# Performance work log

Measured on AMD Instinct MI355X. Metric: run time of the kernel, lower is better.

Reference implementation:

```python
import jax, jax.numpy as jnp
import numpy as np

B, S, H, M = 8, 128, 768, 128
EPS = 1e-12


def setup_inputs() -> dict:
    key = jax.random.key(0)
    ks = jax.random.split(key, 8)
    seq_hiddens = jax.random.normal(ks[0], (B, S, H), dtype=jnp.float32)
    gamma = jnp.ones((H,), jnp.float32)
    beta = jnp.zeros((H,), jnp.float32)
    # conditional LN dense weights (torch Linear weight: (out, in)); small init so math stays stable
    w_beta = jax.random.normal(ks[1], (H, H), dtype=jnp.float32) * 0.02
    w_gamma = jax.random.normal(ks[2], (H, H), dtype=jnp.float32) * 0.02
    w_ent = jax.random.normal(ks[3], (H, M), dtype=jnp.float32) * 0.02
    w_head = jax.random.normal(ks[4], (H, M), dtype=jnp.float32) * 0.02
    w_tail = jax.random.normal(ks[5], (H, M), dtype=jnp.float32) * 0.02
    b_ent = jnp.zeros((M,), jnp.float32)
    b_head = jnp.zeros((M,), jnp.float32)
    b_tail = jnp.zeros((M,), jnp.float32)
    return dict(seq_hiddens=seq_hiddens, gamma=gamma, beta=beta, w_beta=w_beta,
                w_gamma=w_gamma, w_ent=w_ent, b_ent=b_ent, w_head=w_head,
                b_head=b_head, w_tail=w_tail, b_tail=b_tail)


def _handshake_cln(seq, gamma, beta, w_beta, w_gamma):
    # Triangular pair expansion in the same row-major order as the torch loop:
    # for ind in range(S): pairs (ind, ind), (ind, ind+1), ..., (ind, S-1)
    s = seq.shape[1]
    ii, jj = jnp.triu_indices(s)                 # (P,) each, P = S(S+1)/2
    x = seq[:, jj, :]                            # visible hiddens   (B, P, H)
    cond = seq[:, ii, :]                         # repeated hiddens  (B, P, H)
    beta_c = jnp.einsum('bph,oh->bpo', cond, w_beta) + beta      # (B, P, H)
    gamma_c = jnp.einsum('bph,oh->bpo', cond, w_gamma) + gamma   # (B, P, H)
    mean = jnp.mean(x, axis=-1, keepdims=True)
    out = x - mean
    var = jnp.mean(out * out, axis=-1, keepdims=True)
    std = (var + EPS) ** 2                       # NOTE: faithful to source (no sqrt)
    return out / std * gamma_c + beta_c


def reference(seq_hiddens, gamma, beta, w_beta, w_gamma, w_ent, b_ent,
              w_head, b_head, w_tail, b_tail):
    shaking = _handshake_cln(seq_hiddens, gamma, beta, w_beta, w_gamma)  # (B, P, H)
    ent = jnp.tanh(shaking @ w_ent + b_ent)      # (B, P, M)
    head = jnp.tanh(shaking @ w_head + b_head)
    tail = jnp.tanh(shaking @ w_tail + b_tail)
    return jnp.stack([ent, head, tail], axis=0)  # (3, B, P, M)
```

## Files before the change

### kernel.cpp

```cpp
#include <hip/hip_runtime.h>
#include <hip/hip_bf16.h>
#include <hip/hip_fp16.h>
#include <math.h>

#define B_   8
#define S_   128
#define H_   768
#define M_   128
#define P_   8256
#define BP_  66048
#define EPSF 1e-12f

typedef unsigned short u16;
typedef unsigned int   u32;
typedef _Float16 h16;
typedef _Float16 ffrag __attribute__((ext_vector_type(8)));
typedef float    f32x4 __attribute__((ext_vector_type(4)));

__device__ __forceinline__ u32 fuse2(u32 x, u32 g, u32 b) {
    __half2 r = __hfma2(__builtin_bit_cast(__half2, x),
                        __builtin_bit_cast(__half2, g),
                        __builtin_bit_cast(__half2, b));
    return __builtin_bit_cast(u32, r);
}
__device__ __forceinline__ float fast_tanh(float v) {
    float t = __expf(v + v);
    float r = __builtin_amdgcn_rcpf(t + 1.0f);
    return fmaf(-2.0f, r, 1.0f);
}
__device__ __forceinline__ void gl_lds16(const h16* g, h16* l) {
    __builtin_amdgcn_global_load_lds(
        (const __attribute__((address_space(1))) u32*)g,
        (__attribute__((address_space(3))) u32*)l, 16, 0, 0);
}

__global__ void k_prep(const float* __restrict__ seq,
                       const float* __restrict__ wg, const float* __restrict__ wb,
                       const float* __restrict__ we, const float* __restrict__ wh,
                       const float* __restrict__ wt,
                       const float* __restrict__ be, const float* __restrict__ bh,
                       const float* __restrict__ bt,
                       h16* __restrict__ wgb, h16* __restrict__ wbb,
                       h16* __restrict__ wct, float* __restrict__ biasc,
                       h16* __restrict__ xn, h16* __restrict__ condb)
{
    __shared__ float red[4];
    const int bx = blockIdx.x;
    const int t = threadIdx.x;

    if (bx < 5763) {
        int idx = bx * 256 + t;
        if (idx < 589824) {
            wgb[idx] = (h16)wg[idx];
        } else if (idx < 1179648) {
            int i = idx - 589824;
            wbb[i] = (h16)wb[i];
        } else if (idx < 1474560) {
            int i = idx - 1179648;
            int n = i / 768, h = i - n * 768;
            const float* w = (n < 128) ? we : (n < 256 ? wh : wt);
            wct[i] = (h16)w[h * 128 + (n & 127)];
        } else if (idx < 1474944) {
            int n = idx - 1474560;
            biasc[n] = (n < 128) ? be[n] : (n < 256 ? bh[n - 128] : bt[n - 256]);
        }
        return;
    }
    const int row = bx - 5763;
    const int lane = t & 63, wid = t >> 6;
    const float* x = seq + (size_t)row * H_;
    float x0 = x[t], x1 = x[t + 256], x2 = x[t + 512];

    float s = x0 + x1 + x2;
    for (int o = 32; o; o >>= 1) s += __shfl_xor(s, o);
    if (lane == 0) red[wid] = s;
    __syncthreads();
    float mean = (red[0] + red[1] + red[2] + red[3]) * (1.0f / 768.0f);

    float c0 = x0 - mean, c1 = x1 - mean, c2 = x2 - mean;
    float ss = c0 * c0 + c1 * c1 + c2 * c2;
    for (int o = 32; o; o >>= 1) ss += __shfl_xor(ss, o);
    __syncthreads();
    if (lane == 0) red[wid] = ss;
    __syncthreads();
    float var = (red[0] + red[1] + red[2] + red[3]) * (1.0f / 768.0f);
    float sd = var + EPSF;
    float scale = 1.0f / (sd * sd);

    h16* xr = xn + (size_t)row * H_;
    h16* cr = condb + (size_t)row * H_;
    xr[t] = (h16)(c0 * scale); xr[t + 256] = (h16)(c1 * scale); xr[t + 512] = (h16)(c2 * scale);
    cr[t] = (h16)x0;           cr[t + 256] = (h16)x1;           cr[t + 512] = (h16)x2;
}

__global__ __launch_bounds__(256) void k_cond_gemm(
    const h16* __restrict__ Ab, const h16* __restrict__ Wg, const h16* __restrict__ Wb,
    const float* __restrict__ gamma, const float* __restrict__ beta,
    h16* __restrict__ Gc, h16* __restrict__ Bc)
{
    __shared__ h16 Ash[64 * 72];
    __shared__ h16 Bsh[64 * 72];
    const int t = threadIdx.x;
    const int row0 = blockIdx.x * 64;
    const int by = blockIdx.y;
    const bool isg = (by < 12);
    const int nc0 = (isg ? by : by - 12) * 64;
    const h16* wsrc = isg ? Wg : Wb;

    const int r = t >> 2, q = t & 3;
    const h16* ap = Ab + (size_t)(row0 + r) * H_ + q * 16;
    const h16* wp = wsrc + (size_t)(nc0 + r) * H_ + q * 16;
    h16* asto = &Ash[r * 72 + q * 16];
    h16* bsto = &Bsh[r * 72 + q * 16];

    const int lane = t & 63, wid = t >> 6;
    const int wm0 = (wid >> 1) * 32, wn0 = (wid & 1) * 32;
    const int l15 = lane & 15, quad = lane >> 4, q8 = quad * 8;

    f32x4 acc[2][2] = {};
    for (int kt = 0; kt < 12; ++kt) {
        const int k0 = kt * 64;
        uint4 a0 = *(const uint4*)(ap + k0); uint4 a1 = *(const uint4*)(ap + k0 + 8);
        uint4 w0 = *(const uint4*)(wp + k0); uint4 w1 = *(const uint4*)(wp + k0 + 8);
        *(uint4*)asto = a0; *(uint4*)(asto + 8) = a1;
        *(uint4*)bsto = w0; *(uint4*)(bsto + 8) = w1;
        __syncthreads();
#pragma unroll
        for (int ks = 0; ks < 64; ks += 32) {
            ffrag af[2], bf[2];
#pragma unroll
            for (int mi = 0; mi < 2; ++mi)
                af[mi] = *reinterpret_cast<const ffrag*>(&Ash[(wm0 + mi * 16 + l15) * 72 + ks + q8]);
#pragma unroll
            for (int ni = 0; ni < 2; ++ni)
                bf[ni] = *reinterpret_cast<const ffrag*>(&Bsh[(wn0 + ni * 16 + l15) * 72 + ks + q8]);
#pragma unroll
            for (int mi = 0; mi < 2; ++mi)
#pragma unroll
                for (int ni = 0; ni < 2; ++ni)
                    acc[mi][ni] = __builtin_amdgcn_mfma_f32_16x16x32_f16(af[mi], bf[ni], acc[mi][ni], 0, 0, 0);
        }
        __syncthreads();
    }

    const float* bias = isg ? gamma : beta;
    h16* outp = isg ? Gc : Bc;
#pragma unroll
    for (int mi = 0; mi < 2; ++mi)
#pragma unroll
        for (int ni = 0; ni < 2; ++ni) {
            int c = wn0 + ni * 16 + l15;
            float bv = bias[nc0 + c];
#pragma unroll
            for (int reg = 0; reg < 4; ++reg) {
                int rg = wm0 + mi * 16 + quad * 4 + reg;
                outp[(size_t)(row0 + rg) * H_ + nc0 + c] = (h16)(acc[mi][ni][reg] + bv);
            }
        }
}

__global__ __launch_bounds__(256, 2) void k_pair_gemm(
    const h16* __restrict__ Xn, const h16* __restrict__ Gcb, const h16* __restrict__ Bcb,
    const h16* __restrict__ WcT, const float* __restrict__ biasc,
    float* __restrict__ out)
{
    __shared__ h16 Ash[2][4 * 128 * 8];
    __shared__ h16 Bsh[2][4 * 192 * 8];
    __shared__ int offx[128];
    __shared__ int offc[128];

    const int t = threadIdx.x;
    const int row0 = blockIdx.x * 128;
    const int nb = blockIdx.y;

    if (t < 128) {
        int gp = row0 + t;
        int b = gp / P_;
        int p = gp - b * P_;
        int i = (int)((257.0f - sqrtf(66049.0f - 8.0f * (float)p)) * 0.5f);
        if (i < 0) i = 0; if (i > 127) i = 127;
        while (i > 0 && (i * (257 - i)) / 2 > p) --i;
        while (((i + 1) * (256 - i)) / 2 <= p) ++i;
        int j = i + (p - (i * (257 - i)) / 2);
        offx[t] = b * 128 + j;
        offc[t] = b * 128 + i;
    }
    __syncthreads();

    const int r = t >> 1, half = t & 1;
    const h16* xp  = Xn  + (size_t)offx[r] * H_ + half * 16;
    const h16* gp_ = Gcb + (size_t)offc[r] * H_ + half * 16;
    const h16* bp_ = Bcb + (size_t)offc[r] * H_ + half * 16;
    const int aw0 = ((2 * half) * 128 + r) * 8;
    const int aw1 = ((2 * half + 1) * 128 + r) * 8;

    const h16* wbase = WcT + (size_t)nb * 192 * H_;
    const int wud = t & ~63;
    const h16* dsrc[3];
#pragma unroll
    for (int c = 0; c < 3; ++c) {
        int L = c * 256 + t;
        int ch = L / 192, n = L - ch * 192;
        dsrc[c] = wbase + (size_t)n * H_ + ch * 8;
    }

    const int lane = t & 63, wid = t >> 6;
    const int wm0 = (wid >> 1) * 64, wn0 = (wid & 1) * 96;
    const int l15 = lane & 15, quad = lane >> 4;

#pragma unroll
    for (int c = 0; c < 3; ++c)
        gl_lds16(dsrc[c], &Bsh[0][(c * 256 + wud) * 8]);
    {
        uint4 xa = *(const uint4*)xp;   uint4 xb = *(const uint4*)(xp + 8);
        uint4 ga = *(const uint4*)gp_;  uint4 gb = *(const uint4*)(gp_ + 8);
        uint4 ba = *(const uint4*)bp_;  uint4 bb = *(const uint4*)(bp_ + 8);
        uint4 f0, f1;
        f0.x = fuse2(xa.x, ga.x, ba.x); f0.y = fuse2(xa.y, ga.y, ba.y);
        f0.z = fuse2(xa.z, ga.z, ba.z); f0.w = fuse2(xa.w, ga.w, ba.w);
        f1.x = fuse2(xb.x, gb.x, bb.x); f1.y = fuse2(xb.y, gb.y, bb.y);
        f1.z = fuse2(xb.z, gb.z, bb.z); f1.w = fuse2(xb.w, gb.w, bb.w);
        *(uint4*)&Ash[0][aw0] = f0; *(uint4*)&Ash[0][aw1] = f1;
    }
    __syncthreads();

    f32x4 acc[4][6] = {};
#pragma unroll 2
    for (int kt = 0; kt < 24; ++kt) {
        const int buf = kt & 1, nbf = buf ^ 1;
        uint4 xa, xb, ga, gb, ba, bb;
        if (kt < 23) {
            const int k0 = (kt + 1) * 32;
#pragma unroll
            for (int c = 0; c < 3; ++c)
                gl_lds16(dsrc[c] + k0, &Bsh[nbf][(c * 256 + wud) * 8]);
            xa = *(const uint4*)(xp + k0);  xb = *(const uint4*)(xp + k0 + 8);
            ga = *(const uint4*)(gp_ + k0); gb = *(const uint4*)(gp_ + k0 + 8);
            ba = *(const uint4*)(bp_ + k0); bb = *(const uint4*)(bp_ + k0 + 8);
        }

        ffrag af[4], bf[6];
#pragma unroll
        for (int mi = 0; mi < 4; ++mi)
            af[mi] = *reinterpret_cast<const ffrag*>(&Ash[buf][(quad * 128 + wm0 + mi * 16 + l15) * 8]);
#pragma unroll
        for (int ni = 0; ni < 6; ++ni)
            bf[ni] = *reinterpret_cast<const ffrag*>(&Bsh[buf][(quad * 192 + wn0 + ni * 16 + l15) * 8]);
#pragma unroll
        for (int mi = 0; mi < 4; ++mi)
#pragma unroll
            for (int ni = 0; ni < 6; ++ni)
                acc[mi][ni] = __builtin_amdgcn_mfma_f32_16x16x32_f16(af[mi], bf[ni], acc[mi][ni], 0, 0, 0);

        if (kt < 23) {
            uint4 f0, f1;
            f0.x = fuse2(xa.x, ga.x, ba.x); f0.y = fuse2(xa.y, ga.y, ba.y);
            f0.z = fuse2(xa.z, ga.z, ba.z); f0.w = fuse2(xa.w, ga.w, ba.w);
            f1.x = fuse2(xb.x, gb.x, bb.x); f1.y = fuse2(xb.y, gb.y, bb.y);
            f1.z = fuse2(xb.z, gb.z, bb.z); f1.w = fuse2(xb.w, gb.w, bb.w);
            *(uint4*)&Ash[nbf][aw0] = f0; *(uint4*)&Ash[nbf][aw1] = f1;
        }
        __syncthreads();
    }

#pragma unroll
    for (int mi = 0; mi < 4; ++mi)
#pragma unroll
        for (int ni = 0; ni < 6; ++ni) {
            int cg = nb * 192 + wn0 + ni * 16 + l15;
            int head = cg >> 7, m = cg & 127;
            float bv = biasc[cg];
#pragma unroll
            for (int reg = 0; reg < 4; ++reg) {
                int rg = wm0 + mi * 16 + quad * 4 + reg;
                out[((size_t)head * BP_ + row0 + rg) * M_ + m] = fast_tanh(acc[mi][ni][reg] + bv);
            }
        }
}

extern "C" void kernel_launch(void* const* d_in, const int* in_sizes, int n_in,
                              void* d_out, int out_size, void* d_ws, size_t ws_size,
                              hipStream_t stream)
{
    const float* seq     = (const float*)d_in[0];
    const float* gamma   = (const float*)d_in[1];
    const float* beta    = (const float*)d_in[2];
    const float* w_beta  = (const float*)d_in[3];
    const float* w_gamma = (const float*)d_in[4];
    const float* w_ent   = (const float*)d_in[5];
    const float* b_ent   = (const float*)d_in[6];
    const float* w_head  = (const float*)d_in[7];
    const float* b_head  = (const float*)d_in[8];
    const float* w_tail  = (const float*)d_in[9];
    const float* b_tail  = (const float*)d_in[10];
    float* out = (float*)d_out;

    char* ws = (char*)d_ws;
    h16* xn    = (h16*)ws; ws += (size_t)1024 * 768 * 2;
    h16* condb = (h16*)ws; ws += (size_t)1024 * 768 * 2;
    h16* wgb   = (h16*)ws; ws += (size_t)768 * 768 * 2;
    h16* wbb   = (h16*)ws; ws += (size_t)768 * 768 * 2;
    h16* wct   = (h16*)ws; ws += (size_t)384 * 768 * 2;
    h16* gc    = (h16*)ws; ws += (size_t)1024 * 768 * 2;
    h16* bc    = (h16*)ws; ws += (size_t)1024 * 768 * 2;
    float* biasc = (float*)ws; ws += 384 * 4;

    hipLaunchKernelGGL(k_prep, dim3(5763 + 1024), dim3(256), 0, stream,
                       seq, w_gamma, w_beta, w_ent, w_head, w_tail,
                       b_ent, b_head, b_tail, wgb, wbb, wct, biasc, xn, condb);
    hipLaunchKernelGGL(k_cond_gemm, dim3(16, 24), dim3(256), 0, stream,
                       condb, wgb, wbb, gamma, beta, gc, bc);
    hipLaunchKernelGGL(k_pair_gemm, dim3(516, 2), dim3(256), 0, stream,
                       xn, gc, bc, wct, biasc, out);
}
```

Baseline: 234.5 us.

## Halve pair-GEMM row tile to 64 and transpose head weights via LDS

The pair GEMM now uses 64-row tiles, with each of the four waves covering 48 output columns. The grid doubles and launch bounds rise to allow three blocks per CU, which should improve occupancy and load balance across the 256 CUs. In the prep kernel, the strided gather transpose of the head weights is replaced by a 64x64 LDS-tiled transpose so that global reads and writes are coalesced. The cost is less reuse of each B tile and more redundant loads of the weight tiles.

```diff
diff --git a/kernel.cpp b/kernel.cpp
--- a/kernel.cpp
+++ b/kernel.cpp
@@ -34,6 +34,9 @@
         (__attribute__((address_space(3))) u32*)l, 16, 0, 0);
 }
 
+#define CONVN 4610
+#define WCT0  4610
+#define NORM0 4682
 __global__ void k_prep(const float* __restrict__ seq,
                        const float* __restrict__ wg, const float* __restrict__ wb,
                        const float* __restrict__ we, const float* __restrict__ wh,
@@ -45,28 +48,46 @@
                        h16* __restrict__ xn, h16* __restrict__ condb)
 {
     __shared__ float red[4];
+    __shared__ float tile[64][65];
     const int bx = blockIdx.x;
     const int t = threadIdx.x;
 
-    if (bx < 5763) {
+    if (bx < CONVN) {
         int idx = bx * 256 + t;
         if (idx < 589824) {
             wgb[idx] = (h16)wg[idx];
         } else if (idx < 1179648) {
             int i = idx - 589824;
             wbb[i] = (h16)wb[i];
-        } else if (idx < 1474560) {
-            int i = idx - 1179648;
-            int n = i / 768, h = i - n * 768;
-            const float* w = (n < 128) ? we : (n < 256 ? wh : wt);
-            wct[i] = (h16)w[h * 128 + (n & 127)];
-        } else if (idx < 1474944) {
-            int n = idx - 1474560;
+        } else if (idx < 1180032) {
+            int n = idx - 1179648;
             biasc[n] = (n < 128) ? be[n] : (n < 256 ? bh[n - 128] : bt[n - 256]);
         }
         return;
     }
-    const int row = bx - 5763;
+    if (bx < NORM0) {
+        int b = bx - WCT0;
+        int x = b / 24, rem = b - x * 24;
+        int mt = rem / 12, ht = rem - mt * 12;
+        int m0 = mt * 64, h0 = ht * 64;
+        const float* w = (x == 0) ? we : (x == 1 ? wh : wt);
+        int mm = t & 63, hh4 = t >> 6;
+#pragma unroll
+        for (int r2 = 0; r2 < 16; ++r2) {
+            int hh = hh4 + r2 * 4;
+            tile[hh][mm] = w[(size_t)(h0 + hh) * 128 + m0 + mm];
+        }
+        __syncthreads();
+        int hh2 = t & 63, nn4 = t >> 6;
+#pragma unroll
+        for (int r2 = 0; r2 < 16; ++r2) {
+            int nn = nn4 + r2 * 4;
+            int n = x * 128 + m0 + nn;
+            wct[(size_t)n * H_ + h0 + hh2] = (h16)tile[hh2][nn];
+        }
+        return;
+    }
+    const int row = bx - NORM0;
     const int lane = t & 63, wid = t >> 6;
     const float* x = seq + (size_t)row * H_;
     float x0 = x[t], x1 = x[t + 256], x2 = x[t + 512];
@@ -159,21 +180,21 @@
         }
 }
 
-__global__ __launch_bounds__(256, 2) void k_pair_gemm(
+__global__ __launch_bounds__(256, 3) void k_pair_gemm(
     const h16* __restrict__ Xn, const h16* __restrict__ Gcb, const h16* __restrict__ Bcb,
     const h16* __restrict__ WcT, const float* __restrict__ biasc,
     float* __restrict__ out)
 {
-    __shared__ h16 Ash[2][4 * 128 * 8];
+    __shared__ h16 Ash[2][4 * 64 * 8];
     __shared__ h16 Bsh[2][4 * 192 * 8];
-    __shared__ int offx[128];
-    __shared__ int offc[128];
+    __shared__ int offx[64];
+    __shared__ int offc[64];
 
     const int t = threadIdx.x;
-    const int row0 = blockIdx.x * 128;
+    const int row0 = blockIdx.x * 64;
     const int nb = blockIdx.y;
 
-    if (t < 128) {
+    if (t < 64) {
         int gp = row0 + t;
         int b = gp / P_;
         int p = gp - b * P_;
@@ -187,12 +208,11 @@
     }
     __syncthreads();
 
-    const int r = t >> 1, half = t & 1;
-    const h16* xp  = Xn  + (size_t)offx[r] * H_ + half * 16;
-    const h16* gp_ = Gcb + (size_t)offc[r] * H_ + half * 16;
-    const h16* bp_ = Bcb + (size_t)offc[r] * H_ + half * 16;
-    const int aw0 = ((2 * half) * 128 + r) * 8;
-    const int aw1 = ((2 * half + 1) * 128 + r) * 8;
+    const int r = t >> 2, c4 = t & 3;
+    const h16* xp  = Xn  + (size_t)offx[r] * H_ + c4 * 8;
+    const h16* gp_ = Gcb + (size_t)offc[r] * H_ + c4 * 8;
+    const h16* bp_ = Bcb + (size_t)offc[r] * H_ + c4 * 8;
+    const int aw = (c4 * 64 + r) * 8;
 
     const h16* wbase = WcT + (size_t)nb * 192 * H_;
     const int wud = t & ~63;
@@ -205,60 +225,56 @@
     }
 
     const int lane = t & 63, wid = t >> 6;
-    const int wm0 = (wid >> 1) * 64, wn0 = (wid & 1) * 96;
+    const int wn0 = wid * 48;
     const int l15 = lane & 15, quad = lane >> 4;
 
 #pragma unroll
     for (int c = 0; c < 3; ++c)
         gl_lds16(dsrc[c], &Bsh[0][(c * 256 + wud) * 8]);
     {
-        uint4 xa = *(const uint4*)xp;   uint4 xb = *(const uint4*)(xp + 8);
-        uint4 ga = *(const uint4*)gp_;  uint4 gb = *(const uint4*)(gp_ + 8);
-        uint4 ba = *(const uint4*)bp_;  uint4 bb = *(const uint4*)(bp_ + 8);
-        uint4 f0, f1;
-        f0.x = fuse2(xa.x, ga.x, ba.x); f0.y = fuse2(xa.y, ga.y, ba.y);
-        f0.z = fuse2(xa.z, ga.z, ba.z); f0.w = fuse2(xa.w, ga.w, ba.w);
-        f1.x = fuse2(xb.x, gb.x, bb.x); f1.y = fuse2(xb.y, gb.y, bb.y);
-        f1.z = fuse2(xb.z, gb.z, bb.z); f1.w = fuse2(xb.w, gb.w, bb.w);
-        *(uint4*)&Ash[0][aw0] = f0; *(uint4*)&Ash[0][aw1] = f1;
-    }
-    __syncthreads();
-
-    f32x4 acc[4][6] = {};
+        uint4 xa = *(const uint4*)xp;
+        uint4 ga = *(const uint4*)gp_;
+        uint4 ba = *(const uint4*)bp_;
+        uint4 f;
+        f.x = fuse2(xa.x, ga.x, ba.x); f.y = fuse2(xa.y, ga.y, ba.y);
+        f.z = fuse2(xa.z, ga.z, ba.z); f.w = fuse2(xa.w, ga.w, ba.w);
+        *(uint4*)&Ash[0][aw] = f;
+    }
+    __syncthreads();
+
+    f32x4 acc[4][3] = {};
 #pragma unroll 2
     for (int kt = 0; kt < 24; ++kt) {
         const int buf = kt & 1, nbf = buf ^ 1;
-        uint4 xa, xb, ga, gb, ba, bb;
+        uint4 xa, ga, ba;
         if (kt < 23) {
             const int k0 = (kt + 1) * 32;
 #pragma unroll
             for (int c = 0; c < 3; ++c)
                 gl_lds16(dsrc[c] + k0, &Bsh[nbf][(c * 256 + wud) * 8]);
-            xa = *(const uint4*)(xp + k0);  xb = *(const uint4*)(xp + k0 + 8);
-            ga = *(const uint4*)(gp_ + k0); gb = *(const uint4*)(gp_ + k0 + 8);
-            ba = *(const uint4*)(bp_ + k0); bb = *(const uint4*)(bp_ + k0 + 8);
-        }
-
-        ffrag af[4], bf[6];
+            xa = *(const uint4*)(xp + k0);
+            ga = *(const uint4*)(gp_ + k0);
+            ba = *(const uint4*)(bp_ + k0);
+        }
+
+        ffrag af[4], bf[3];
 #pragma unroll
         for (int mi = 0; mi < 4; ++mi)
-            af[mi] = *reinterpret_cast<const ffrag*>(&Ash[buf][(quad * 128 + wm0 + mi * 16 + l15) * 8]);
-#pragma unroll
-        for (int ni = 0; ni < 6; ++ni)
+            af[mi] = *reinterpret_cast<const ffrag*>(&Ash[buf][(quad * 64 + mi * 16 + l15) * 8]);
+#pragma unroll
+        for (int ni = 0; ni < 3; ++ni)
             bf[ni] = *reinterpret_cast<const ffrag*>(&Bsh[buf][(quad * 192 + wn0 + ni * 16 + l15) * 8]);
 #pragma unroll
         for (int mi = 0; mi < 4; ++mi)
 #pragma unroll
-            for (int ni = 0; ni < 6; ++ni)
+            for (int ni = 0; ni < 3; ++ni)
                 acc[mi][ni] = __builtin_amdgcn_mfma_f32_16x16x32_f16(af[mi], bf[ni], acc[mi][ni], 0, 0, 0);
 
         if (kt < 23) {
-            uint4 f0, f1;
-            f0.x = fuse2(xa.x, ga.x, ba.x); f0.y = fuse2(xa.y, ga.y, ba.y);
-            f0.z = fuse2(xa.z, ga.z, ba.z); f0.w = fuse2(xa.w, ga.w, ba.w);
-            f1.x = fuse2(xb.x, gb.x, bb.x); f1.y = fuse2(xb.y, gb.y, bb.y);
-            f1.z = fuse2(xb.z, gb.z, bb.z); f1.w = fuse2(xb.w, gb.w, bb.w);
-            *(uint4*)&Ash[nbf][aw0] = f0; *(uint4*)&Ash[nbf][aw1] = f1;
+            uint4 f;
+            f.x = fuse2(xa.x, ga.x, ba.x); f.y = fuse2(xa.y, ga.y, ba.y);
+            f.z = fuse2(xa.z, ga.z, ba.z); f.w = fuse2(xa.w, ga.w, ba.w);
+            *(uint4*)&Ash[nbf][aw] = f;
         }
         __syncthreads();
     }
@@ -266,13 +282,13 @@
 #pragma unroll
     for (int mi = 0; mi < 4; ++mi)
 #pragma unroll
-        for (int ni = 0; ni < 6; ++ni) {
+        for (int ni = 0; ni < 3; ++ni) {
             int cg = nb * 192 + wn0 + ni * 16 + l15;
             int head = cg >> 7, m = cg & 127;
             float bv = biasc[cg];
 #pragma unroll
             for (int reg = 0; reg < 4; ++reg) {
-                int rg = wm0 + mi * 16 + quad * 4 + reg;
+                int rg = mi * 16 + quad * 4 + reg;
                 out[((size_t)head * BP_ + row0 + rg) * M_ + m] = fast_tanh(acc[mi][ni][reg] + bv);
             }
         }
@@ -305,11 +321,11 @@
     h16* bc    = (h16*)ws; ws += (size_t)1024 * 768 * 2;
     float* biasc = (float*)ws; ws += 384 * 4;
 
-    hipLaunchKernelGGL(k_prep, dim3(5763 + 1024), dim3(256), 0, stream,
+    hipLaunchKernelGGL(k_prep, dim3(NORM0 + 1024), dim3(256), 0, stream,
                        seq, w_gamma, w_beta, w_ent, w_head, w_tail,
                        b_ent, b_head, b_tail, wgb, wbb, wct, biasc, xn, condb);
     hipLaunchKernelGGL(k_cond_gemm, dim3(16, 24), dim3(256), 0, stream,
                        condb, wgb, wbb, gamma, beta, gc, bc);
-    hipLaunchKernelGGL(k_pair_gemm, dim3(516, 2), dim3(256), 0, stream,
+    hipLaunchKernelGGL(k_pair_gemm, dim3(1032, 2), dim3(256), 0, stream,
                        xn, gc, bc, wct, biasc, out);
 }
```

Result: slower. 250.3 us (+6.7%).

## Pre-pack output weights into tile order and shrink pair-GEMM row tile

Applied to the files above, without the earlier changes.

The head weights are now pre-packed in the prep kernel into a tile-contiguous layout, so each k-step's weight tile is one contiguous 24KB chunk loaded straight to LDS. The pair GEMM switches from 128x192 tiles with K-step 32 to 64x192 tiles with K-step 64, doubling the grid to 1032x2 blocks and halving the k-loop trips. The aim is more blocks for occupancy and load balance on the GPU, plus fewer barriers and simpler weight addressing. The cost is that each weight tile is reused by fewer rows, so weight traffic per output row roughly doubles.

```diff
diff --git a/kernel.cpp b/kernel.cpp
--- a/kernel.cpp
+++ b/kernel.cpp
@@ -34,6 +34,7 @@
         (__attribute__((address_space(3))) u32*)l, 16, 0, 0);
 }
 
+#define NORM0 5763
 __global__ void k_prep(const float* __restrict__ seq,
                        const float* __restrict__ wg, const float* __restrict__ wb,
                        const float* __restrict__ we, const float* __restrict__ wh,
@@ -41,14 +42,14 @@
                        const float* __restrict__ be, const float* __restrict__ bh,
                        const float* __restrict__ bt,
                        h16* __restrict__ wgb, h16* __restrict__ wbb,
-                       h16* __restrict__ wct, float* __restrict__ biasc,
+                       h16* __restrict__ wpk, float* __restrict__ biasc,
                        h16* __restrict__ xn, h16* __restrict__ condb)
 {
     __shared__ float red[4];
     const int bx = blockIdx.x;
     const int t = threadIdx.x;
 
-    if (bx < 5763) {
+    if (bx < NORM0) {
         int idx = bx * 256 + t;
         if (idx < 589824) {
             wgb[idx] = (h16)wg[idx];
@@ -57,16 +58,26 @@
             wbb[i] = (h16)wb[i];
         } else if (idx < 1474560) {
             int i = idx - 1179648;
-            int n = i / 768, h = i - n * 768;
-            const float* w = (n < 128) ? we : (n < 256 ? wh : wt);
-            wct[i] = (h16)w[h * 128 + (n & 127)];
+            int e  = i & 7;
+            int u  = i >> 3;
+            int n  = u % 192;
+            int v  = u / 192;
+            int ch = v & 7;
+            int w2 = v >> 3;
+            int kt = w2 % 12;
+            int nb = w2 / 12;
+            int h  = kt * 64 + ch * 8 + e;
+            int ng = nb * 192 + n;
+            int head = ng >> 7, m = ng & 127;
+            const float* src = (head == 0) ? we : (head == 1 ? wh : wt);
+            wpk[i] = (h16)src[h * 128 + m];
         } else if (idx < 1474944) {
             int n = idx - 1474560;
             biasc[n] = (n < 128) ? be[n] : (n < 256 ? bh[n - 128] : bt[n - 256]);
         }
         return;
     }
-    const int row = bx - 5763;
+    const int row = bx - NORM0;
     const int lane = t & 63, wid = t >> 6;
     const float* x = seq + (size_t)row * H_;
     float x0 = x[t], x1 = x[t + 256], x2 = x[t + 512];
@@ -161,19 +172,19 @@
 
 __global__ __launch_bounds__(256, 2) void k_pair_gemm(
     const h16* __restrict__ Xn, const h16* __restrict__ Gcb, const h16* __restrict__ Bcb,
-    const h16* __restrict__ WcT, const float* __restrict__ biasc,
+    const h16* __restrict__ Wpk, const float* __restrict__ biasc,
     float* __restrict__ out)
 {
-    __shared__ h16 Ash[2][4 * 128 * 8];
-    __shared__ h16 Bsh[2][4 * 192 * 8];
-    __shared__ int offx[128];
-    __shared__ int offc[128];
+    __shared__ h16 Ash[2][8 * 64 * 8];
+    __shared__ h16 Bsh[2][8 * 192 * 8];
+    __shared__ int offx[64];
+    __shared__ int offc[64];
 
     const int t = threadIdx.x;
-    const int row0 = blockIdx.x * 128;
+    const int row0 = blockIdx.x * 64;
     const int nb = blockIdx.y;
 
-    if (t < 128) {
+    if (t < 64) {
         int gp = row0 + t;
         int b = gp / P_;
         int p = gp - b * P_;
@@ -187,30 +198,23 @@
     }
     __syncthreads();
 
-    const int r = t >> 1, half = t & 1;
-    const h16* xp  = Xn  + (size_t)offx[r] * H_ + half * 16;
-    const h16* gp_ = Gcb + (size_t)offc[r] * H_ + half * 16;
-    const h16* bp_ = Bcb + (size_t)offc[r] * H_ + half * 16;
-    const int aw0 = ((2 * half) * 128 + r) * 8;
-    const int aw1 = ((2 * half + 1) * 128 + r) * 8;
-
-    const h16* wbase = WcT + (size_t)nb * 192 * H_;
+    const int r = t >> 2, c4 = t & 3;
+    const h16* xp  = Xn  + (size_t)offx[r] * H_ + c4 * 16;
+    const h16* gp_ = Gcb + (size_t)offc[r] * H_ + c4 * 16;
+    const h16* bp_ = Bcb + (size_t)offc[r] * H_ + c4 * 16;
+    const int aw0 = ((2 * c4) * 64 + r) * 8;
+    const int aw1 = ((2 * c4 + 1) * 64 + r) * 8;
+
+    const h16* wtile = Wpk + (size_t)nb * 12 * 12288;
     const int wud = t & ~63;
-    const h16* dsrc[3];
-#pragma unroll
-    for (int c = 0; c < 3; ++c) {
-        int L = c * 256 + t;
-        int ch = L / 192, n = L - ch * 192;
-        dsrc[c] = wbase + (size_t)n * H_ + ch * 8;
-    }
 
     const int lane = t & 63, wid = t >> 6;
-    const int wm0 = (wid >> 1) * 64, wn0 = (wid & 1) * 96;
+    const int wn0 = wid * 48;
     const int l15 = lane & 15, quad = lane >> 4;
 
 #pragma unroll
-    for (int c = 0; c < 3; ++c)
-        gl_lds16(dsrc[c], &Bsh[0][(c * 256 + wud) * 8]);
+    for (int c = 0; c < 6; ++c)
+        gl_lds16(wtile + (size_t)(c * 256 + t) * 8, &Bsh[0][(c * 256 + wud) * 8]);
     {
         uint4 xa = *(const uint4*)xp;   uint4 xb = *(const uint4*)(xp + 8);
         uint4 ga = *(const uint4*)gp_;  uint4 gb = *(const uint4*)(gp_ + 8);
@@ -224,35 +228,42 @@
     }
     __syncthreads();
 
-    f32x4 acc[4][6] = {};
+    f32x4 acc[4][3] = {};
 #pragma unroll 2
-    for (int kt = 0; kt < 24; ++kt) {
+    for (int kt = 0; kt < 12; ++kt) {
         const int buf = kt & 1, nbf = buf ^ 1;
         uint4 xa, xb, ga, gb, ba, bb;
-        if (kt < 23) {
-            const int k0 = (kt + 1) * 32;
-#pragma unroll
-            for (int c = 0; c < 3; ++c)
-                gl_lds16(dsrc[c] + k0, &Bsh[nbf][(c * 256 + wud) * 8]);
+        if (kt < 11) {
+            const h16* wnext = wtile + (size_t)(kt + 1) * 12288;
+#pragma unroll
+            for (int c = 0; c < 6; ++c)
+                gl_lds16(wnext + (size_t)(c * 256 + t) * 8, &Bsh[nbf][(c * 256 + wud) * 8]);
+            const int k0 = (kt + 1) * 64;
             xa = *(const uint4*)(xp + k0);  xb = *(const uint4*)(xp + k0 + 8);
             ga = *(const uint4*)(gp_ + k0); gb = *(const uint4*)(gp_ + k0 + 8);
             ba = *(const uint4*)(bp_ + k0); bb = *(const uint4*)(bp_ + k0 + 8);
         }
 
-        ffrag af[4], bf[6];
-#pragma unroll
-        for (int mi = 0; mi < 4; ++mi)
-            af[mi] = *reinterpret_cast<const ffrag*>(&Ash[buf][(quad * 128 + wm0 + mi * 16 + l15) * 8]);
-#pragma unroll
-        for (int ni = 0; ni < 6; ++ni)
-            bf[ni] = *reinterpret_cast<const ffrag*>(&Bsh[buf][(quad * 192 + wn0 + ni * 16 + l15) * 8]);
-#pragma unroll
-        for (int mi = 0; mi < 4; ++mi)
-#pragma unroll
-            for (int ni = 0; ni < 6; ++ni)
-                acc[mi][ni] = __builtin_amdgcn_mfma_f32_16x16x32_f16(af[mi], bf[ni], acc[mi][ni], 0, 0, 0);
-
-        if (kt < 23) {
+#pragma unroll
+        for (int ks = 0; ks < 64; ks += 32) {
+            const int ch0 = ks >> 3;
+            ffrag af[4], bf[3];
+#pragma unroll
+            for (int mi = 0; mi < 4; ++mi)
+                af[mi] = *reinterpret_cast<const ffrag*>(
+                    &Ash[buf][((ch0 + quad) * 64 + mi * 16 + l15) * 8]);
+#pragma unroll
+            for (int ni = 0; ni < 3; ++ni)
+                bf[ni] = *reinterpret_cast<const ffrag*>(
+                    &Bsh[buf][((ch0 + quad) * 192 + wn0 + ni * 16 + l15) * 8]);
+#pragma unroll
+            for (int mi = 0; mi < 4; ++mi)
+#pragma unroll
+                for (int ni = 0; ni < 3; ++ni)
+                    acc[mi][ni] = __builtin_amdgcn_mfma_f32_16x16x32_f16(af[mi], bf[ni], acc[mi][ni], 0, 0, 0);
+        }
+
+        if (kt < 11) {
             uint4 f0, f1;
             f0.x = fuse2(xa.x, ga.x, ba.x); f0.y = fuse2(xa.y, ga.y, ba.y);
             f0.z = fuse2(xa.z, ga.z, ba.z); f0.w = fuse2(xa.w, ga.w, ba.w);
@@ -266,13 +277,13 @@
 #pragma unroll
     for (int mi = 0; mi < 4; ++mi)
 #pragma unroll
-        for (int ni = 0; ni < 6; ++ni) {
+        for (int ni = 0; ni < 3; ++ni) {
             int cg = nb * 192 + wn0 + ni * 16 + l15;
             int head = cg >> 7, m = cg & 127;
             float bv = biasc[cg];
 #pragma unroll
             for (int reg = 0; reg < 4; ++reg) {
-                int rg = wm0 + mi * 16 + quad * 4 + reg;
+                int rg = mi * 16 + quad * 4 + reg;
                 out[((size_t)head * BP_ + row0 + rg) * M_ + m] = fast_tanh(acc[mi][ni][reg] + bv);
             }
         }
@@ -300,16 +311,16 @@
     h16* condb = (h16*)ws; ws += (size_t)1024 * 768 * 2;
     h16* wgb   = (h16*)ws; ws += (size_t)768 * 768 * 2;
     h16* wbb   = (h16*)ws; ws += (size_t)768 * 768 * 2;
-    h16* wct   = (h16*)ws; ws += (size_t)384 * 768 * 2;
+    h16* wpk   = (h16*)ws; ws += (size_t)294912 * 2;
     h16* gc    = (h16*)ws; ws += (size_t)1024 * 768 * 2;
     h16* bc    = (h16*)ws; ws += (size_t)1024 * 768 * 2;
     float* biasc = (float*)ws; ws += 384 * 4;
 
-    hipLaunchKernelGGL(k_prep, dim3(5763 + 1024), dim3(256), 0, stream,
+    hipLaunchKernelGGL(k_prep, dim3(NORM0 + 1024), dim3(256), 0, stream,
                        seq, w_gamma, w_beta, w_ent, w_head, w_tail,
-                       b_ent, b_head, b_tail, wgb, wbb, wct, biasc, xn, condb);
+                       b_ent, b_head, b_tail, wgb, wbb, wpk, biasc, xn, condb);
     hipLaunchKernelGGL(k_cond_gemm, dim3(16, 24), dim3(256), 0, stream,
                        condb, wgb, wbb, gamma, beta, gc, bc);
-    hipLaunchKernelGGL(k_pair_gemm, dim3(516, 2), dim3(256), 0, stream,
-                       xn, gc, bc, wct, biasc, out);
-}
+    hipLaunchKernelGGL(k_pair_gemm, dim3(1032, 2), dim3(256), 0, stream,
+                       xn, gc, bc, wpk, biasc, out);
+}
```

Result: faster. 212.6 us (-9.4%).
